# Optimization experiments

Measured on AMD Instinct MI355X. Metric: run time of the kernel, lower is better.

Reference implementation:

```python
import jax, jax.numpy as jnp
import numpy as np

N_G = 100000  # gene nodes
N_T = 100000  # trait nodes
E = 500000    # edges per etype
D_IN = 128
D_OUT = 128


def setup_inputs() -> dict:
    key = jax.random.key(0)
    ks = jax.random.split(key, 20)
    inp = {
        "x_gene": jax.random.normal(ks[0], (N_G, D_IN), jnp.float32),
        "x_trait": jax.random.normal(ks[1], (N_T, D_IN), jnp.float32),
        "src_gg": jax.random.randint(ks[2], (E,), 0, N_G, jnp.int32),
        "dst_gg": jax.random.randint(ks[3], (E,), 0, N_G, jnp.int32),
        "src_gt": jax.random.randint(ks[4], (E,), 0, N_G, jnp.int32),
        "dst_gt": jax.random.randint(ks[5], (E,), 0, N_T, jnp.int32),
        "src_tg": jax.random.randint(ks[6], (E,), 0, N_T, jnp.int32),
        "dst_tg": jax.random.randint(ks[7], (E,), 0, N_G, jnp.int32),
    }
    # one SAGEConv per edge type: W_neigh, W_self [D_IN, D_OUT], bias [D_OUT]
    i = 8
    for et in ("gg", "gt", "tg"):
        inp[f"Wn_{et}"] = jax.random.normal(ks[i], (D_IN, D_OUT), jnp.float32) * 0.05; i += 1
        inp[f"Ws_{et}"] = jax.random.normal(ks[i], (D_IN, D_OUT), jnp.float32) * 0.05; i += 1
        inp[f"b_{et}"] = jnp.zeros((D_OUT,), jnp.float32)
    return inp


def _sage(x_src, x_dst, src, dst, Wn, Ws, b, n_dst):
    # DGL SAGEConv with 'mean' aggregator:
    # h_neigh = mean over in-edges of src features (0 if no in-edges)
    msg = x_src[src]                                   # [E, D_IN] gather
    ssum = jax.ops.segment_sum(msg, dst, num_segments=n_dst)      # [n_dst, D_IN]
    deg = jax.ops.segment_sum(jnp.ones((src.shape[0],), x_src.dtype), dst,
                              num_segments=n_dst)
    h_neigh = ssum / jnp.maximum(deg, 1.0)[:, None]
    return x_dst @ Ws + h_neigh @ Wn + b               # [n_dst, D_OUT]


def reference(x_gene, x_trait, src_gg, dst_gg, src_gt, dst_gt, src_tg, dst_tg,
              Wn_gg, Ws_gg, b_gg, Wn_gt, Ws_gt, b_gt, Wn_tg, Ws_tg, b_tg):
    h_gg = _sage(x_gene, x_gene, src_gg, dst_gg, Wn_gg, Ws_gg, b_gg, N_G)
    h_gt = _sage(x_gene, x_trait, src_gt, dst_gt, Wn_gt, Ws_gt, b_gt, N_T)
    h_tg = _sage(x_trait, x_gene, src_tg, dst_tg, Wn_tg, Ws_tg, b_tg, N_G)
    # h_node accumulation: gene is dst of both gg and tg
    h_gene = h_gg + h_tg
    h_trait = h_gt
    return (h_gene, h_trait)
```

## Files before the change

### kernel.cpp

```cpp
#include <hip/hip_runtime.h>
#include <hip/hip_bf16.h>


#define D 128
#define NG 100000
#define NT 100000
#define NSEG (NG + NT + NG)

#define NBUCK 256
#define NPB   ((NSEG + NBUCK - 1) / NBUCK)
#define TILE  4096
#define CAP   8192
#define CAPW  128

typedef __bf16 bf16x8 __attribute__((ext_vector_type(8)));
typedef float f32x16 __attribute__((ext_vector_type(16)));
typedef float v2f __attribute__((ext_vector_type(2)));

static __device__ __forceinline__ unsigned short f2bf(float f) {
    return __builtin_bit_cast(unsigned short, (__bf16)f);
}
static __device__ __forceinline__ float bflo(unsigned int v) {
    return __builtin_bit_cast(float, v << 16);
}
static __device__ __forceinline__ float bfhi(unsigned int v) {
    return __builtin_bit_cast(float, v & 0xffff0000u);
}

static __device__ __forceinline__ int edge_seg(
    int ge, const int* d0, int n0, const int* d1, int n1, const int* d2)
{
    if (ge < n0) return d0[ge];
    if (ge < n0 + n1) return NG + d1[ge - n0];
    return NG + NT + d2[ge - n0 - n1];
}
static __device__ __forceinline__ int edge_src(
    int ge, const int* s0, int n0, const int* s1, int n1, const int* s2)
{
    if (ge < n0) return s0[ge];
    if (ge < n0 + n1) return s1[ge - n0];
    return s2[ge - n0 - n1];
}

#define CVT8 (((NG + 1) + (NT + 1)) * D / 8)
#define SETUP_ITEMS (CVT8 + 6144 + 4096 + 128 + 128)

__global__ __launch_bounds__(256) void setup_scatter_kernel(
    const int* __restrict__ s0, const int* __restrict__ d0, int n0,
    const int* __restrict__ s1, const int* __restrict__ d1, int n1,
    const int* __restrict__ s2, const int* __restrict__ d2, int nE,
    int* __restrict__ cellcnt, int2* __restrict__ binned, int nWG,
    const float* __restrict__ xg, const float* __restrict__ xt,
    unsigned short* __restrict__ og, unsigned short* __restrict__ ot,
    const float* __restrict__ Ws_gg, const float* __restrict__ Ws_tg,
    const float* __restrict__ Wn_gg, const float* __restrict__ Wn_tg,
    const float* __restrict__ Ws_gt, const float* __restrict__ Wn_gt,
    const float* __restrict__ b_gg, const float* __restrict__ b_tg,
    const float* __restrict__ b_gt,
    unsigned short* __restrict__ WpG, unsigned short* __restrict__ WpT,
    float* __restrict__ biasG, float* __restrict__ biasT)
{
    __shared__ int2 stage[TILE];
    __shared__ int hist[NBUCK], scn[NBUCK], lcur[NBUCK];
    const int t = threadIdx.x;

    if ((int)blockIdx.x < nWG) {
        hist[t] = 0;
        __syncthreads();

        const int base = blockIdx.x * TILE;
        int mseg[TILE / 256], msrc[TILE / 256];
#pragma unroll
        for (int j = 0; j < TILE / 256; ++j) {
            const int ge = base + j * 256 + t;
            if (ge < nE) {
                mseg[j] = edge_seg(ge, d0, n0, d1, n1, d2);
                msrc[j] = edge_src(ge, s0, n0, s1, n1, s2);
                atomicAdd(&hist[mseg[j] / NPB], 1);
            } else mseg[j] = -1;
        }
        __syncthreads();

        const int h = hist[t];
        cellcnt[(size_t)t * nWG + blockIdx.x] = min(h, CAPW);

        scn[t] = h;
        __syncthreads();
        for (int sh = 1; sh < NBUCK; sh <<= 1) {
            int u = (t >= sh) ? scn[t - sh] : 0;
            __syncthreads();
            scn[t] += u;
            __syncthreads();
        }
        const int excl = scn[t] - h;
        __syncthreads();
        scn[t] = excl;
        lcur[t] = excl;
        __syncthreads();

#pragma unroll
        for (int j = 0; j < TILE / 256; ++j) {
            if (mseg[j] >= 0) {
                const int b = mseg[j] / NPB;
                const int pos = atomicAdd(&lcur[b], 1);
                stage[pos] = make_int2(msrc[j], mseg[j]);
            }
        }
        __syncthreads();

        const int cnt = min(TILE, nE - base);
        for (int slot = t; slot < cnt; slot += 256) {
            const int2 pr = stage[slot];
            const int b = pr.y / NPB;
            const int pic = slot - scn[b];
            if (pic < CAPW)
                binned[((size_t)b * nWG + blockIdx.x) * CAPW + pic] = pr;
        }
        return;
    }

    const int gid = (blockIdx.x - nWG) * 256 + t;
    if (gid < CVT8) {
        const int ng8 = (NG + 1) * D / 8;
        const float* x; unsigned short* o; int j, nreal8;
        if (gid < ng8) { x = xg; o = og; j = gid;       nreal8 = NG * D / 8; }
        else           { x = xt; o = ot; j = gid - ng8; nreal8 = NT * D / 8; }
        uint4 v = make_uint4(0, 0, 0, 0);
        if (j < nreal8) {
            const float4 f0 = ((const float4*)x)[j * 2];
            const float4 f1 = ((const float4*)x)[j * 2 + 1];
            v.x = (unsigned int)f2bf(f0.x) | ((unsigned int)f2bf(f0.y) << 16);
            v.y = (unsigned int)f2bf(f0.z) | ((unsigned int)f2bf(f0.w) << 16);
            v.z = (unsigned int)f2bf(f1.x) | ((unsigned int)f2bf(f1.y) << 16);
            v.w = (unsigned int)f2bf(f1.z) | ((unsigned int)f2bf(f1.w) << 16);
        }
        ((uint4*)o)[j] = v;
        return;
    }
    const int g2 = gid - CVT8;
    if (g2 < 6144) {
        const int lane = g2 & 63, nt = (g2 >> 6) & 3, kt = g2 >> 8;
        const int n = nt * 32 + (lane & 31);
        const int kb = kt * 16 + (lane >> 5) * 8;
        unsigned int pk[4];
#pragma unroll
        for (int jj = 0; jj < 4; ++jj) {
            unsigned int w2 = 0;
#pragma unroll
            for (int h = 0; h < 2; ++h) {
                const int k = kb + jj * 2 + h;
                float w;
                if (k < 128)      w = Ws_gg[k * D + n] + Ws_tg[k * D + n];
                else if (k < 256) w = Wn_gg[(k - 128) * D + n];
                else              w = Wn_tg[(k - 256) * D + n];
                w2 |= ((unsigned int)f2bf(w)) << (16 * h);
            }
            pk[jj] = w2;
        }
        *(uint4*)(WpG + (size_t)g2 * 8) = make_uint4(pk[0], pk[1], pk[2], pk[3]);
    } else if (g2 < 6144 + 4096) {
        const int g = g2 - 6144;
        const int lane = g & 63, nt = (g >> 6) & 3, kt = g >> 8;
        const int n = nt * 32 + (lane & 31);
        const int kb = kt * 16 + (lane >> 5) * 8;
        unsigned int pk[4];
#pragma unroll
        for (int jj = 0; jj < 4; ++jj) {
            unsigned int w2 = 0;
#pragma unroll
            for (int h = 0; h < 2; ++h) {
                const int k = kb + jj * 2 + h;
                const float w = (k < 128) ? Ws_gt[k * D + n] : Wn_gt[(k - 128) * D + n];
                w2 |= ((unsigned int)f2bf(w)) << (16 * h);
            }
            pk[jj] = w2;
        }
        *(uint4*)(WpT + (size_t)g * 8) = make_uint4(pk[0], pk[1], pk[2], pk[3]);
    } else if (g2 < 10240 + 128) {
        const int i = g2 - 10240;
        biasG[i] = b_gg[i] + b_tg[i];
    } else if (g2 < 10368 + 128) {
        const int i = g2 - 10368;
        biasT[i] = b_gt[i];
    }
}

__global__ __launch_bounds__(256) void bbuild_kernel(
    const int2* __restrict__ binned, const int* __restrict__ cellcnt, int nWG,
    int* __restrict__ off, int* __restrict__ dend, int* __restrict__ sorted)
{
    constexpr int CH = (NPB + 255) / 256;
    __shared__ int ldeg[NPB];
    __shared__ int loff[NPB];
    __shared__ int psum[256];
    const int t = threadIdx.x;
    const int b = blockIdx.x;
    const int n0 = b * NPB;
    const int NL = min(NSEG - n0, NPB);

    for (int i = t; i < NL; i += 256) ldeg[i] = 0;
    __syncthreads();

    for (int w = t; w < nWG; w += 256) {
        const int c = min(cellcnt[(size_t)b * nWG + w], CAPW);
        const int2* cell = binned + ((size_t)b * nWG + w) * CAPW;
        for (int i = 0; i < c; ++i)
            atomicAdd(&ldeg[cell[i].y - n0], 1);
    }
    __syncthreads();

    int s = 0;
#pragma unroll
    for (int k = 0; k < CH; ++k) {
        const int i = t * CH + k;
        if (i < NL) s += ldeg[i];
    }
    psum[t] = s;
    __syncthreads();
    for (int sh = 1; sh < 256; sh <<= 1) {
        int u = (t >= sh) ? psum[t - sh] : 0;
        __syncthreads();
        psum[t] += u;
        __syncthreads();
    }
    int run = psum[t] - s;
#pragma unroll
    for (int k = 0; k < CH; ++k) {
        const int i = t * CH + k;
        if (i < NL) { loff[i] = run; run += ldeg[i]; }
    }
    __syncthreads();

    const int ebase = b * CAP;
    for (int i = t; i < NL; i += 256) {
        off[n0 + i]  = ebase + loff[i];
        dend[n0 + i] = ebase + loff[i] + ldeg[i];
    }
    __syncthreads();

    for (int w = t; w < nWG; w += 256) {
        const int c = min(cellcnt[(size_t)b * nWG + w], CAPW);
        const int2* cell = binned + ((size_t)b * nWG + w) * CAPW;
        for (int i = 0; i < c; ++i) {
            const int2 pr = cell[i];
            const int slot = atomicAdd(&loff[pr.y - n0], 1);
            sorted[ebase + slot] = pr.x;
        }
    }
}

__global__ __launch_bounds__(256) void agg_all_kernel(
    const unsigned short* __restrict__ xg, const unsigned short* __restrict__ xt,
    const int* __restrict__ off, const int* __restrict__ dend,
    const int* __restrict__ sorted,
    unsigned short* __restrict__ aggA, unsigned short* __restrict__ aggC,
    unsigned short* __restrict__ aggB)
{
    const int t = threadIdx.x;
    const int node = blockIdx.x * 16 + (t >> 4);
    if (node >= NSEG) return;
    const int l = t & 15;
    const int gb = (t & 63) & ~15;
    const int s0 = off[node];
    const int s1 = dend[node];

    const unsigned short* xb;
    unsigned short* out;
    int local, zrow;
    if (node < NG)           { xb = xg; out = aggA; local = node;           zrow = NG; }
    else if (node < NG + NT) { xb = xg; out = aggC; local = node - NG;      zrow = NG; }
    else                     { xb = xt; out = aggB; local = node - NG - NT; zrow = NT; }

    v2f A0 = (v2f){0.f, 0.f}, A1 = (v2f){0.f, 0.f};
    v2f A2 = (v2f){0.f, 0.f}, A3 = (v2f){0.f, 0.f};

    for (int e = s0; e < s1; e += 16) {
        const int cnt = min(s1 - e, 16);
        const int myidx = sorted[e + min(l, cnt - 1)];
#pragma unroll
        for (int j = 0; j < 16; j += 4) {
            if (j < cnt) {
                const int i0 = __shfl(myidx, gb + j, 64);
                const int i1 = (j + 1 < cnt) ? __shfl(myidx, gb + j + 1, 64) : zrow;
                const int i2 = (j + 2 < cnt) ? __shfl(myidx, gb + j + 2, 64) : zrow;
                const int i3 = (j + 3 < cnt) ? __shfl(myidx, gb + j + 3, 64) : zrow;
                const uint4 v0 = *(const uint4*)(xb + (size_t)i0 * D + l * 8);
                const uint4 v1 = *(const uint4*)(xb + (size_t)i1 * D + l * 8);
                const uint4 v2 = *(const uint4*)(xb + (size_t)i2 * D + l * 8);
                const uint4 v3 = *(const uint4*)(xb + (size_t)i3 * D + l * 8);
                A0 += (v2f){bflo(v0.x), bfhi(v0.x)};
                A1 += (v2f){bflo(v0.y), bfhi(v0.y)};
                A2 += (v2f){bflo(v0.z), bfhi(v0.z)};
                A3 += (v2f){bflo(v0.w), bfhi(v0.w)};
                A0 += (v2f){bflo(v1.x), bfhi(v1.x)};
                A1 += (v2f){bflo(v1.y), bfhi(v1.y)};
                A2 += (v2f){bflo(v1.z), bfhi(v1.z)};
                A3 += (v2f){bflo(v1.w), bfhi(v1.w)};
                A0 += (v2f){bflo(v2.x), bfhi(v2.x)};
                A1 += (v2f){bflo(v2.y), bfhi(v2.y)};
                A2 += (v2f){bflo(v2.z), bfhi(v2.z)};
                A3 += (v2f){bflo(v2.w), bfhi(v2.w)};
                A0 += (v2f){bflo(v3.x), bfhi(v3.x)};
                A1 += (v2f){bflo(v3.y), bfhi(v3.y)};
                A2 += (v2f){bflo(v3.z), bfhi(v3.z)};
                A3 += (v2f){bflo(v3.w), bfhi(v3.w)};
            }
        }
    }

    const float inv = 1.0f / (float)max(s1 - s0, 1);
    uint4 o;
    o.x = (unsigned int)f2bf(A0.x * inv) | ((unsigned int)f2bf(A0.y * inv) << 16);
    o.y = (unsigned int)f2bf(A1.x * inv) | ((unsigned int)f2bf(A1.y * inv) << 16);
    o.z = (unsigned int)f2bf(A2.x * inv) | ((unsigned int)f2bf(A2.y * inv) << 16);
    o.w = (unsigned int)f2bf(A3.x * inv) | ((unsigned int)f2bf(A3.y * inv) << 16);
    *(uint4*)(out + (size_t)local * D + l * 8) = o;
}

__global__ __launch_bounds__(512) void gemm_all(
    const unsigned short* __restrict__ xbG, const unsigned short* __restrict__ xbT,
    const unsigned short* __restrict__ aggA, const unsigned short* __restrict__ aggB,
    const unsigned short* __restrict__ aggC,
    const unsigned short* __restrict__ WpG, const unsigned short* __restrict__ WpT,
    const float* __restrict__ biasG, const float* __restrict__ biasT,
    float* __restrict__ outG, float* __restrict__ outT, int GB)
{
    const int t = threadIdx.x;
    const int wid = t >> 6, lane = t & 63;
    const int lm = lane & 31, l5 = lane >> 5;

    const bool isG = (int)blockIdx.x < GB;
    const int bloc = isG ? blockIdx.x : blockIdx.x - GB;
    const int M = isG ? NG : NT;
    const int nsrc = isG ? 3 : 2;
    const unsigned short* A0 = isG ? xbG : xbT;
    const unsigned short* A1 = isG ? aggA : aggC;
    const unsigned short* A2 = aggB;
    const unsigned short* Wpack = isG ? WpG : WpT;
    const float* bias = isG ? biasG : biasT;
    float* out = isG ? outG : outT;

    const int tile = bloc * 8 + wid;
    if (tile * 32 >= M) return;
    const int m = tile * 32 + lm;

    f32x16 acc[4];
#pragma unroll
    for (int nt = 0; nt < 4; ++nt) {
#pragma unroll
        for (int q = 0; q < 4; ++q) {
            const float4 bq = *(const float4*)&bias[nt * 32 + 4 * l5 + 8 * q];
            acc[nt][4 * q + 0] = bq.x; acc[nt][4 * q + 1] = bq.y;
            acc[nt][4 * q + 2] = bq.z; acc[nt][4 * q + 3] = bq.w;
        }
    }

#pragma unroll 1
    for (int s = 0; s < nsrc; ++s) {
        const unsigned short* ag = (s == 0) ? A0 : ((s == 1) ? A1 : A2);
        const unsigned short* ar = ag + (size_t)m * D + l5 * 8;
        const unsigned short* wbase = Wpack + (size_t)s * (8 * 4 * 64 * 8) + (size_t)lane * 8;
#pragma unroll
        for (int kt = 0; kt < 8; ++kt) {
            const bf16x8 a = *(const bf16x8*)(ar + kt * 16);
#pragma unroll
            for (int nt = 0; nt < 4; ++nt) {
                const bf16x8 b = *(const bf16x8*)(wbase + (size_t)(kt * 4 + nt) * 64 * 8);
                acc[nt] = __builtin_amdgcn_mfma_f32_32x32x16_bf16(b, a, acc[nt], 0, 0, 0);
            }
        }
    }

    float* orow = out + (size_t)m * D;
#pragma unroll
    for (int nt = 0; nt < 4; ++nt) {
        float* p = orow + nt * 32 + 4 * l5;
        *(float4*)(p + 0)  = make_float4(acc[nt][0],  acc[nt][1],  acc[nt][2],  acc[nt][3]);
        *(float4*)(p + 8)  = make_float4(acc[nt][4],  acc[nt][5],  acc[nt][6],  acc[nt][7]);
        *(float4*)(p + 16) = make_float4(acc[nt][8],  acc[nt][9],  acc[nt][10], acc[nt][11]);
        *(float4*)(p + 24) = make_float4(acc[nt][12], acc[nt][13], acc[nt][14], acc[nt][15]);
    }
}

extern "C" void kernel_launch(void* const* d_in, const int* in_sizes, int n_in,
                              void* d_out, int out_size, void* d_ws, size_t ws_size,
                              hipStream_t stream)
{
    const float* x_gene  = (const float*)d_in[0];
    const float* x_trait = (const float*)d_in[1];
    const int* src_gg = (const int*)d_in[2];
    const int* dst_gg = (const int*)d_in[3];
    const int* src_gt = (const int*)d_in[4];
    const int* dst_gt = (const int*)d_in[5];
    const int* src_tg = (const int*)d_in[6];
    const int* dst_tg = (const int*)d_in[7];
    const float* Wn_gg = (const float*)d_in[8];
    const float* Ws_gg = (const float*)d_in[9];
    const float* b_gg  = (const float*)d_in[10];
    const float* Wn_gt = (const float*)d_in[11];
    const float* Ws_gt = (const float*)d_in[12];
    const float* b_gt  = (const float*)d_in[13];
    const float* Wn_tg = (const float*)d_in[14];
    const float* Ws_tg = (const float*)d_in[15];
    const float* b_tg  = (const float*)d_in[16];

    const int nE_gg = in_sizes[2];
    const int nE_gt = in_sizes[4];
    const int nE_tg = in_sizes[6];
    const int nE_total = nE_gg + nE_gt + nE_tg;
    const int nWG = (nE_total + TILE - 1) / TILE;

    float* out_gene  = (float*)d_out;
    float* out_trait = (float*)d_out + (size_t)NG * D;

    unsigned short* xb_gene  = (unsigned short*)d_ws;
    unsigned short* xb_trait = xb_gene + (size_t)(NG + 1) * D;
    unsigned short* aggA = xb_trait + (size_t)(NT + 1) * D;
    unsigned short* aggB = aggA + (size_t)NG * D;
    unsigned short* aggC = aggB + (size_t)NG * D;
    char* p = (char*)(aggC + (size_t)NT * D);
    unsigned short* WpG = (unsigned short*)p;  p += 24 * 4 * 64 * 8 * sizeof(unsigned short);
    unsigned short* WpT = (unsigned short*)p;  p += 16 * 4 * 64 * 8 * sizeof(unsigned short);
    float* biasG = (float*)p;                  p += D * sizeof(float);
    float* biasT = (float*)p;                  p += D * sizeof(float);
    int* off     = (int*)p;                    p += (size_t)NSEG * sizeof(int);
    int* dend    = (int*)p;                    p += (size_t)NSEG * sizeof(int);
    int* sorted  = (int*)p;                    p += (size_t)NBUCK * CAP * sizeof(int);
    int* cellcnt = (int*)p;                    p += (size_t)NBUCK * nWG * sizeof(int);
    int2* binned = (int2*)p;

    const int setup_blocks = (SETUP_ITEMS + 255) / 256;
    setup_scatter_kernel<<<nWG + setup_blocks, 256, 0, stream>>>(
        src_gg, dst_gg, nE_gg, src_gt, dst_gt, nE_gt, src_tg, dst_tg,
        nE_total, cellcnt, binned, nWG,
        x_gene, x_trait, xb_gene, xb_trait,
        Ws_gg, Ws_tg, Wn_gg, Wn_tg, Ws_gt, Wn_gt, b_gg, b_tg, b_gt,
        WpG, WpT, biasG, biasT);

    bbuild_kernel<<<NBUCK, 256, 0, stream>>>(binned, cellcnt, nWG, off, dend, sorted);

    agg_all_kernel<<<(NSEG + 15) / 16, 256, 0, stream>>>(
        xb_gene, xb_trait, off, dend, sorted, aggA, aggC, aggB);

    const int GBb = ((NG + 31) / 32 + 7) / 8;
    const int TBb = ((NT + 31) / 32 + 7) / 8;
    gemm_all<<<GBb + TBb, 512, 0, stream>>>(
        xb_gene, xb_trait, aggA, aggB, aggC, WpG, WpT, biasG, biasT,
        out_gene, out_trait, GBb);
}
```

Measured before the change: 181.6 us.

## Fuse neighbor-mean aggregation into GEMM via LDS tiles

Replaces the separate aggregation kernel and GEMM kernel with a single kernel. Each block gathers 32-node mean rows into shared memory and then runs the MFMA GEMM from LDS, with each of four waves computing one 32-column slice. This removes the global write and re-read of the bf16 aggregate buffers and one kernel launch. In exchange, only half the waves do GEMM work, gene tiles run two gathers serially, and the tile counts assume NG and NT divide by 32.

Result: no change. 183.9 us (+1.3%).

```diff
diff --git a/kernel.cpp b/kernel.cpp
--- a/kernel.cpp
+++ b/kernel.cpp
@@ -12,6 +12,7 @@
 #define TILE  4096
 #define CAP   8192
 #define CAPW  128
+#define LROW  136
 
 typedef __bf16 bf16x8 __attribute__((ext_vector_type(8)));
 typedef float f32x16 __attribute__((ext_vector_type(16)));
@@ -249,27 +250,17 @@
     }
 }
 
-__global__ __launch_bounds__(256) void agg_all_kernel(
-    const unsigned short* __restrict__ xg, const unsigned short* __restrict__ xt,
-    const int* __restrict__ off, const int* __restrict__ dend,
-    const int* __restrict__ sorted,
-    unsigned short* __restrict__ aggA, unsigned short* __restrict__ aggC,
-    unsigned short* __restrict__ aggB)
-{
-    const int t = threadIdx.x;
-    const int node = blockIdx.x * 16 + (t >> 4);
-    if (node >= NSEG) return;
+static __device__ __forceinline__ void gather_to_lds(
+    const unsigned short* __restrict__ xb, const int* __restrict__ off,
+    const int* __restrict__ dend, const int* __restrict__ sorted,
+    int segbase, int tile, int t, unsigned short* lds, int zrow)
+{
+    const int g = t >> 4;
     const int l = t & 15;
     const int gb = (t & 63) & ~15;
+    const int node = segbase + tile * 32 + g;
     const int s0 = off[node];
     const int s1 = dend[node];
-
-    const unsigned short* xb;
-    unsigned short* out;
-    int local, zrow;
-    if (node < NG)           { xb = xg; out = aggA; local = node;           zrow = NG; }
-    else if (node < NG + NT) { xb = xg; out = aggC; local = node - NG;      zrow = NG; }
-    else                     { xb = xt; out = aggB; local = node - NG - NT; zrow = NT; }
 
     v2f A0 = (v2f){0.f, 0.f}, A1 = (v2f){0.f, 0.f};
     v2f A2 = (v2f){0.f, 0.f}, A3 = (v2f){0.f, 0.f};
@@ -314,72 +305,68 @@
     o.y = (unsigned int)f2bf(A1.x * inv) | ((unsigned int)f2bf(A1.y * inv) << 16);
     o.z = (unsigned int)f2bf(A2.x * inv) | ((unsigned int)f2bf(A2.y * inv) << 16);
     o.w = (unsigned int)f2bf(A3.x * inv) | ((unsigned int)f2bf(A3.y * inv) << 16);
-    *(uint4*)(out + (size_t)local * D + l * 8) = o;
-}
-
-__global__ __launch_bounds__(512) void gemm_all(
+    *(uint4*)(lds + (size_t)g * LROW + l * 8) = o;
+}
+
+__global__ __launch_bounds__(512) void fused_agg_gemm(
     const unsigned short* __restrict__ xbG, const unsigned short* __restrict__ xbT,
-    const unsigned short* __restrict__ aggA, const unsigned short* __restrict__ aggB,
-    const unsigned short* __restrict__ aggC,
+    const int* __restrict__ off, const int* __restrict__ dend,
+    const int* __restrict__ sorted,
     const unsigned short* __restrict__ WpG, const unsigned short* __restrict__ WpT,
     const float* __restrict__ biasG, const float* __restrict__ biasT,
     float* __restrict__ outG, float* __restrict__ outT, int GB)
 {
+    __shared__ unsigned short MEAN[2][32 * LROW];
     const int t = threadIdx.x;
-    const int wid = t >> 6, lane = t & 63;
+    const bool isG = (int)blockIdx.x < GB;
+    const int tile = isG ? blockIdx.x : blockIdx.x - GB;
+
+    if (isG) {
+        gather_to_lds(xbG, off, dend, sorted, 0,       tile, t, MEAN[0], NG);
+        gather_to_lds(xbT, off, dend, sorted, NG + NT, tile, t, MEAN[1], NT);
+    } else {
+        gather_to_lds(xbG, off, dend, sorted, NG,      tile, t, MEAN[0], NG);
+    }
+    __syncthreads();
+
+    const int wid = t >> 6;
+    if (wid >= 4) return;
+    const int lane = t & 63;
     const int lm = lane & 31, l5 = lane >> 5;
-
-    const bool isG = (int)blockIdx.x < GB;
-    const int bloc = isG ? blockIdx.x : blockIdx.x - GB;
-    const int M = isG ? NG : NT;
-    const int nsrc = isG ? 3 : 2;
-    const unsigned short* A0 = isG ? xbG : xbT;
-    const unsigned short* A1 = isG ? aggA : aggC;
-    const unsigned short* A2 = aggB;
+    const int nt = wid;
+    const int m = tile * 32 + lm;
+
+    const unsigned short* self  = isG ? xbG : xbT;
     const unsigned short* Wpack = isG ? WpG : WpT;
     const float* bias = isG ? biasG : biasT;
     float* out = isG ? outG : outT;
-
-    const int tile = bloc * 8 + wid;
-    if (tile * 32 >= M) return;
-    const int m = tile * 32 + lm;
-
-    f32x16 acc[4];
-#pragma unroll
-    for (int nt = 0; nt < 4; ++nt) {
-#pragma unroll
-        for (int q = 0; q < 4; ++q) {
-            const float4 bq = *(const float4*)&bias[nt * 32 + 4 * l5 + 8 * q];
-            acc[nt][4 * q + 0] = bq.x; acc[nt][4 * q + 1] = bq.y;
-            acc[nt][4 * q + 2] = bq.z; acc[nt][4 * q + 3] = bq.w;
-        }
-    }
-
+    const int nkt = isG ? 24 : 16;
+
+    f32x16 acc;
+#pragma unroll
+    for (int q = 0; q < 4; ++q) {
+        const float4 bq = *(const float4*)&bias[nt * 32 + 4 * l5 + 8 * q];
+        acc[4 * q + 0] = bq.x; acc[4 * q + 1] = bq.y;
+        acc[4 * q + 2] = bq.z; acc[4 * q + 3] = bq.w;
+    }
+
+    const unsigned short* ar = self + (size_t)m * D + l5 * 8;
+    const unsigned short* wb = Wpack + (size_t)lane * 8 + (size_t)nt * 64 * 8;
 #pragma unroll 1
-    for (int s = 0; s < nsrc; ++s) {
-        const unsigned short* ag = (s == 0) ? A0 : ((s == 1) ? A1 : A2);
-        const unsigned short* ar = ag + (size_t)m * D + l5 * 8;
-        const unsigned short* wbase = Wpack + (size_t)s * (8 * 4 * 64 * 8) + (size_t)lane * 8;
-#pragma unroll
-        for (int kt = 0; kt < 8; ++kt) {
-            const bf16x8 a = *(const bf16x8*)(ar + kt * 16);
-#pragma unroll
-            for (int nt = 0; nt < 4; ++nt) {
-                const bf16x8 b = *(const bf16x8*)(wbase + (size_t)(kt * 4 + nt) * 64 * 8);
-                acc[nt] = __builtin_amdgcn_mfma_f32_32x32x16_bf16(b, a, acc[nt], 0, 0, 0);
-            }
-        }
-    }
-
-    float* orow = out + (size_t)m * D;
-#pragma unroll
-    for (int nt = 0; nt < 4; ++nt) {
-        float* p = orow + nt * 32 + 4 * l5;
-        *(float4*)(p + 0)  = make_float4(acc[nt][0],  acc[nt][1],  acc[nt][2],  acc[nt][3]);
-        *(float4*)(p + 8)  = make_float4(acc[nt][4],  acc[nt][5],  acc[nt][6],  acc[nt][7]);
-        *(float4*)(p + 16) = make_float4(acc[nt][8],  acc[nt][9],  acc[nt][10], acc[nt][11]);
-        *(float4*)(p + 24) = make_float4(acc[nt][12], acc[nt][13], acc[nt][14], acc[nt][15]);
-    }
+    for (int kt = 0; kt < nkt; ++kt) {
+        bf16x8 a;
+        if (kt < 8)       a = *(const bf16x8*)(ar + kt * 16);
+        else if (kt < 16) a = *(const bf16x8*)&MEAN[0][(size_t)lm * LROW + (kt - 8) * 16 + l5 * 8];
+        else              a = *(const bf16x8*)&MEAN[1][(size_t)lm * LROW + (kt - 16) * 16 + l5 * 8];
+        const bf16x8 b = *(const bf16x8*)(wb + (size_t)kt * 4 * 64 * 8);
+        acc = __builtin_amdgcn_mfma_f32_32x32x16_bf16(b, a, acc, 0, 0, 0);
+    }
+
+    float* p = out + (size_t)m * D + nt * 32 + 4 * l5;
+    *(float4*)(p + 0)  = make_float4(acc[0],  acc[1],  acc[2],  acc[3]);
+    *(float4*)(p + 8)  = make_float4(acc[4],  acc[5],  acc[6],  acc[7]);
+    *(float4*)(p + 16) = make_float4(acc[8],  acc[9],  acc[10], acc[11]);
+    *(float4*)(p + 24) = make_float4(acc[12], acc[13], acc[14], acc[15]);
 }
 
 extern "C" void kernel_launch(void* const* d_in, const int* in_sizes, int n_in,
@@ -415,10 +402,7 @@
 
     unsigned short* xb_gene  = (unsigned short*)d_ws;
     unsigned short* xb_trait = xb_gene + (size_t)(NG + 1) * D;
-    unsigned short* aggA = xb_trait + (size_t)(NT + 1) * D;
-    unsigned short* aggB = aggA + (size_t)NG * D;
-    unsigned short* aggC = aggB + (size_t)NG * D;
-    char* p = (char*)(aggC + (size_t)NT * D);
+    char* p = (char*)(xb_trait + (size_t)(NT + 1) * D);
     unsigned short* WpG = (unsigned short*)p;  p += 24 * 4 * 64 * 8 * sizeof(unsigned short);
     unsigned short* WpT = (unsigned short*)p;  p += 16 * 4 * 64 * 8 * sizeof(unsigned short);
     float* biasG = (float*)p;                  p += D * sizeof(float);
@@ -439,12 +423,9 @@
 
     bbuild_kernel<<<NBUCK, 256, 0, stream>>>(binned, cellcnt, nWG, off, dend, sorted);
 
-    agg_all_kernel<<<(NSEG + 15) / 16, 256, 0, stream>>>(
-        xb_gene, xb_trait, off, dend, sorted, aggA, aggC, aggB);
-
-    const int GBb = ((NG + 31) / 32 + 7) / 8;
-    const int TBb = ((NT + 31) / 32 + 7) / 8;
-    gemm_all<<<GBb + TBb, 512, 0, stream>>>(
-        xb_gene, xb_trait, aggA, aggB, aggC, WpG, WpT, biasG, biasT,
+    const int GBb = NG / 32;
+    const int TBb = NT / 32;
+    fused_agg_gemm<<<GBb + TBb, 512, 0, stream>>>(
+        xb_gene, xb_trait, off, dend, sorted, WpG, WpT, biasG, biasT,
         out_gene, out_trait, GBb);
 }
```
